# Kernel optimization log

Hardware: AMD Instinct MI355X
Metric: run time of the kernel (lower is better)

The kernel has to match this reference:

```python
import jax, jax.numpy as jnp
import numpy as np

B, L, D = 16, 2048, 256

def setup_inputs() -> dict:
    key = jax.random.key(0)
    k1, k2 = jax.random.split(key)
    inp = jax.random.normal(k1, (B, L, D), dtype=jnp.float32)
    # Linear(2*dim, 1, bias=False) weight, torch layout [out=1, in=2*dim]
    v_w = jax.random.normal(k2, (1, 2 * D), dtype=jnp.float32) * (1.0 / np.sqrt(2 * D))
    return {"inp": inp, "v_w": v_w}


def reference(inp, v_w):
    # score[b,i,j] = cat(query=inp[b,i], key=inp[b,j]) . v_w
    # decomposes exactly into two rank-1 projections broadcast-summed.
    dim = inp.shape[-1]
    wq = v_w[0, :dim]   # multiplies the query half (unsqueeze(1) -> index i)
    wk = v_w[0, dim:]   # multiplies the key half (unsqueeze(2) -> index j)
    sq = jnp.einsum('bld,d->bl', inp, wq)          # [B,L]
    sk = jnp.einsum('bld,d->bl', inp, wk)          # [B,L]
    score = sq[:, :, None] + sk[:, None, :]        # [B,L,L]
    attn = jax.nn.softmax(score, axis=2)           # Softmax(2)
    out = jnp.einsum('bij,bjd->bid', attn, inp)    # bmm
    return (out, attn)
```

## Files before the change

kernel.cpp:

```cpp
#include <hip/hip_runtime.h>

#define BB 16
#define LL 2048
#define DD 256

typedef float vf4 __attribute__((ext_vector_type(4)));

__global__ void __launch_bounds__(256)
k1_pass(const float* __restrict__ inp, const float* __restrict__ wk,
        float* __restrict__ e, float* __restrict__ upart, float* __restrict__ zpart) {
    const int t = threadIdx.x, lane = t & 63, wid = t >> 6;
    const int blk = blockIdx.x;
    const int row0 = blk * 16 + wid * 4;

    const float4 w = *reinterpret_cast<const float4*>(wk + lane * 4);
    float4 acc = make_float4(0.f, 0.f, 0.f, 0.f);
    float zsum = 0.f;

    #pragma unroll
    for (int r = 0; r < 4; ++r) {
        const int row = row0 + r;
        const float4 a = *reinterpret_cast<const float4*>(inp + (size_t)row * DD + lane * 4);
        float dot = a.x * w.x + a.y * w.y + a.z * w.z + a.w * w.w;
        #pragma unroll
        for (int off = 32; off >= 1; off >>= 1) dot += __shfl_xor(dot, off, 64);
        const float ev = __expf(dot);
        if (lane == 0) e[row] = ev;
        zsum += ev;
        acc.x = fmaf(ev, a.x, acc.x);
        acc.y = fmaf(ev, a.y, acc.y);
        acc.z = fmaf(ev, a.z, acc.z);
        acc.w = fmaf(ev, a.w, acc.w);
    }

    __shared__ float uacc[4][DD];
    __shared__ float zw[4];
    *reinterpret_cast<float4*>(&uacc[wid][lane * 4]) = acc;
    if (lane == 0) zw[wid] = zsum;
    __syncthreads();
    float u = uacc[0][t] + uacc[1][t] + uacc[2][t] + uacc[3][t];
    upart[(size_t)blk * DD + t] = u;
    if (t == 0) zpart[blk] = zw[0] + zw[1] + zw[2] + zw[3];
}

__global__ void __launch_bounds__(256)
k2_finalize(const float* __restrict__ upart, const float* __restrict__ zpart,
            const float* __restrict__ e, float* __restrict__ p,
            float* __restrict__ out_vec) {
    const int b = blockIdx.x, t = threadIdx.x;
    __shared__ float zs[128];
    __shared__ float Zsh;
    if (t < 128) zs[t] = zpart[b * 128 + t];
    __syncthreads();
    if (t == 0) {
        float z = 0.f;
        #pragma unroll 8
        for (int i = 0; i < 128; ++i) z += zs[i];
        Zsh = z;
    }
    __syncthreads();
    const float invZ = 1.0f / Zsh;

    float acc = 0.f;
    #pragma unroll 8
    for (int c = 0; c < 128; ++c) acc += upart[((size_t)(b * 128 + c)) * DD + t];
    out_vec[b * DD + t] = acc * invZ;

    #pragma unroll
    for (int r = 0; r < 8; ++r) {
        int j = r * 256 + t;
        p[b * LL + j] = e[b * LL + j] * invZ;
    }
}

__global__ void __launch_bounds__(256)
k3_write(const vf4* __restrict__ outv4, const vf4* __restrict__ p4,
         vf4* __restrict__ dst) {
    const size_t OUT4 = (size_t)BB * LL * DD / 4;
    const size_t TOT4 = OUT4 + (size_t)BB * LL * LL / 4;
    const size_t stride = (size_t)gridDim.x * blockDim.x;
    for (size_t i = blockIdx.x * (size_t)blockDim.x + threadIdx.x; i < TOT4; i += stride) {
        vf4 v;
        if (i < OUT4) {
            size_t b  = i >> 17;
            size_t d4 = i & 63;
            v = outv4[(b << 6) + d4];
        } else {
            size_t k  = i - OUT4;
            size_t b  = k >> 20;
            size_t j4 = k & 511;
            v = p4[(b << 9) + j4];
        }
        __builtin_nontemporal_store(v, &dst[i]);
    }
}

extern "C" void kernel_launch(void* const* d_in, const int* in_sizes, int n_in,
                              void* d_out, int out_size, void* d_ws, size_t ws_size,
                              hipStream_t stream) {
    const float* inp = (const float*)d_in[0];
    const float* vw  = (const float*)d_in[1];
    float* out = (float*)d_out;
    float* ws  = (float*)d_ws;

    float* e       = ws;
    float* upart   = ws + 32768;
    float* zpart   = ws + 557056;
    float* p       = ws + 559104;
    float* out_vec = ws + 591872;

    k1_pass    <<<2048, 256, 0, stream>>>(inp, vw + DD, e, upart, zpart);
    k2_finalize<<<BB,   256, 0, stream>>>(upart, zpart, e, p, out_vec);
    k3_write   <<<2048, 256, 0, stream>>>((const vf4*)out_vec, (const vf4*)p,
                                          (vf4*)out);
}
```

Baseline: 72.46 us.

## Fuse finalize into write kernel, computing normalizers redundantly per block

Removes the 16-block finalize kernel by folding the Z reduction and the output-vector reduction into the final write kernel. Every block recomputes all 16 inverse normalizers from the partial sums. 256 blocks each reduce one batch's upart and broadcast the resulting row over their slice of the output. The remaining blocks scale e by invZ on the fly while streaming the attention matrix. This saves a launch and a serial low-occupancy stage, at the cost of redundant reads of upart (each batch is reduced 16 times) and some load imbalance between block roles.

```diff
diff --git a/kernel.cpp b/kernel.cpp
--- a/kernel.cpp
+++ b/kernel.cpp
@@ -3,11 +3,15 @@
 #define BB 16
 #define LL 2048
 #define DD 256
+#define D1B 2048
+#define OUTB 256
+#define D2B 2048
+#define ATTB (D2B - OUTB)
 
 typedef float vf4 __attribute__((ext_vector_type(4)));
 
 __global__ void __launch_bounds__(256)
-k1_pass(const float* __restrict__ inp, const float* __restrict__ wk,
+d1_pass(const float* __restrict__ inp, const float* __restrict__ wk,
         float* __restrict__ e, float* __restrict__ upart, float* __restrict__ zpart) {
     const int t = threadIdx.x, lane = t & 63, wid = t >> 6;
     const int blk = blockIdx.x;
@@ -38,60 +42,62 @@
     *reinterpret_cast<float4*>(&uacc[wid][lane * 4]) = acc;
     if (lane == 0) zw[wid] = zsum;
     __syncthreads();
-    float u = uacc[0][t] + uacc[1][t] + uacc[2][t] + uacc[3][t];
-    upart[(size_t)blk * DD + t] = u;
+    upart[(size_t)blk * DD + t] = uacc[0][t] + uacc[1][t] + uacc[2][t] + uacc[3][t];
     if (t == 0) zpart[blk] = zw[0] + zw[1] + zw[2] + zw[3];
 }
 
 __global__ void __launch_bounds__(256)
-k2_finalize(const float* __restrict__ upart, const float* __restrict__ zpart,
-            const float* __restrict__ e, float* __restrict__ p,
-            float* __restrict__ out_vec) {
-    const int b = blockIdx.x, t = threadIdx.x;
-    __shared__ float zs[128];
-    __shared__ float Zsh;
-    if (t < 128) zs[t] = zpart[b * 128 + t];
-    __syncthreads();
-    if (t == 0) {
-        float z = 0.f;
-        #pragma unroll 8
-        for (int i = 0; i < 128; ++i) z += zs[i];
-        Zsh = z;
+d2_write(const float* __restrict__ upart, const float* __restrict__ zpart,
+         const float* __restrict__ e, float* __restrict__ out) {
+    const int blk = blockIdx.x, t = threadIdx.x;
+    __shared__ float zs[256];
+    __shared__ float invZ[BB];
+    {
+        int b = t >> 4, c = t & 15;
+        const float* zp = zpart + b * 128 + c * 8;
+        float s = 0.f;
+        #pragma unroll
+        for (int i = 0; i < 8; ++i) s += zp[i];
+        zs[t] = s;
     }
     __syncthreads();
-    const float invZ = 1.0f / Zsh;
+    if (t < BB) {
+        float z = 0.f;
+        #pragma unroll
+        for (int c = 0; c < 16; ++c) z += zs[t * 16 + c];
+        invZ[t] = 1.0f / z;
+    }
+    __syncthreads();
 
-    float acc = 0.f;
-    #pragma unroll 8
-    for (int c = 0; c < 128; ++c) acc += upart[((size_t)(b * 128 + c)) * DD + t];
-    out_vec[b * DD + t] = acc * invZ;
+    const size_t OUT4 = (size_t)BB * LL * DD / 4;
+    vf4* dst4 = (vf4*)out;
 
-    #pragma unroll
-    for (int r = 0; r < 8; ++r) {
-        int j = r * 256 + t;
-        p[b * LL + j] = e[b * LL + j] * invZ;
-    }
-}
-
-__global__ void __launch_bounds__(256)
-k3_write(const vf4* __restrict__ outv4, const vf4* __restrict__ p4,
-         vf4* __restrict__ dst) {
-    const size_t OUT4 = (size_t)BB * LL * DD / 4;
-    const size_t TOT4 = OUT4 + (size_t)BB * LL * LL / 4;
-    const size_t stride = (size_t)gridDim.x * blockDim.x;
-    for (size_t i = blockIdx.x * (size_t)blockDim.x + threadIdx.x; i < TOT4; i += stride) {
-        vf4 v;
-        if (i < OUT4) {
-            size_t b  = i >> 17;
-            size_t d4 = i & 63;
-            v = outv4[(b << 6) + d4];
-        } else {
-            size_t k  = i - OUT4;
-            size_t b  = k >> 20;
-            size_t j4 = k & 511;
-            v = p4[(b << 9) + j4];
+    if (blk < OUTB) {
+        const int b = blk >> 4;
+        const float* up = upart + ((size_t)b * 128) * DD + t;
+        float acc = 0.f;
+        #pragma unroll 8
+        for (int c = 0; c < 128; ++c) acc += up[(size_t)c * DD];
+        __shared__ float ov[DD];
+        ov[t] = acc * invZ[b];
+        __syncthreads();
+        const vf4* ovv = (const vf4*)ov;
+        vf4* dst = dst4 + (size_t)blk * 8192;
+        #pragma unroll 4
+        for (int it = 0; it < 32; ++it) {
+            int idx = it * 256 + t;
+            __builtin_nontemporal_store(ovv[idx & 63], &dst[idx]);
         }
-        __builtin_nontemporal_store(v, &dst[i]);
+    } else {
+        const vf4* e4 = (const vf4*)e;
+        const size_t ATT4 = (size_t)BB * LL * LL / 4;
+        const size_t stride = (size_t)ATTB * 256;
+        for (size_t k = (size_t)(blk - OUTB) * 256 + t; k < ATT4; k += stride) {
+            size_t b = k >> 20, j4 = k & 511;
+            vf4 v = e4[(b << 9) + j4];
+            v *= invZ[b];
+            __builtin_nontemporal_store(v, &dst4[OUT4 + k]);
+        }
     }
 }
 
@@ -103,14 +109,10 @@
     float* out = (float*)d_out;
     float* ws  = (float*)d_ws;
 
-    float* e       = ws;
-    float* upart   = ws + 32768;
-    float* zpart   = ws + 557056;
-    float* p       = ws + 559104;
-    float* out_vec = ws + 591872;
+    float* e     = ws;
+    float* upart = ws + 32768;
+    float* zpart = ws + 557056;
 
-    k1_pass    <<<2048, 256, 0, stream>>>(inp, vw + DD, e, upart, zpart);
-    k2_finalize<<<BB,   256, 0, stream>>>(upart, zpart, e, p, out_vec);
-    k3_write   <<<2048, 256, 0, stream>>>((const vf4*)out_vec, (const vf4*)p,
-                                          (vf4*)out);
+    d1_pass <<<D1B, 256, 0, stream>>>(inp, vw + DD, e, upart, zpart);
+    d2_write<<<D2B, 256, 0, stream>>>(upart, zpart, e, out);
 }
```

Result: faster. 65.64 us (median of 2 runs) (-9.4%).
